# Performance work log

Hardware: AMD Instinct MI355X
Metric: run time of the kernel (lower is better)

The kernel has to match this reference:

```python
import jax, jax.numpy as jnp
import numpy as np

STDDEV = 8.0

def setup_inputs() -> dict:
    key = jax.random.key(0)
    k1, k2, k3, k4 = jax.random.split(key, 4)
    B, S, D, O = 32, 4096, 1024, 1024
    source_hidden_sequence = jax.random.normal(k1, (B, S, D), dtype=jnp.float32)
    target_hidden = jax.random.normal(k2, (B, D), dtype=jnp.float32)
    positions = jax.random.randint(k3, (B,), 0, S, dtype=jnp.int32)
    attention_weights = jax.random.normal(k4, (D + D, O), dtype=jnp.float32) * 0.02
    return {
        "source_hidden_sequence": source_hidden_sequence,
        "target_hidden": target_hidden,
        "positions": positions,
        "attention_weights": attention_weights,
    }

def reference(source_hidden_sequence, target_hidden, positions, attention_weights):
    # source_hidden_sequence: [B, S, D]; target_hidden: [B, D]; positions: [B]
    S = source_hidden_sequence.shape[1]
    # dot-product score per source position: [B, S]
    score = jnp.einsum('bsd,bd->bs', source_hidden_sequence, target_hidden)
    weights = jax.nn.softmax(score, axis=1)
    # Gaussian local-position decay centered at positions
    rel = jnp.arange(S, dtype=jnp.float32)[None, :] - positions.astype(jnp.float32)[:, None]  # [B, S]
    pos_w = jnp.exp(-(rel * rel) / (2.0 * STDDEV * STDDEV))
    weights = weights * pos_w
    # weighted sum over source sequence: [B, D]
    weighted = jnp.einsum('bsd,bs->bd', source_hidden_sequence, weights)
    combined = jnp.concatenate([target_hidden, weighted], axis=1)  # [B, 2D]
    return jnp.tanh(combined @ attention_weights)
```

## Files before the change

### kernel.cpp

```cpp
#include <hip/hip_runtime.h>

#define BB 32
#define SS 4096
#define DD 1024
#define OO 1024
#define KK 2048
#define RAD 64
#define NSPLIT 8

__global__ __launch_bounds__(256) void k_score(const float* __restrict__ src,
                                               const float* __restrict__ tgt,
                                               float* __restrict__ score) {
  const int b = blockIdx.y;
  const int wave = threadIdx.x >> 6;
  const int lane = threadIdx.x & 63;
  const int s_base = blockIdx.x * 16 + wave * 4;
  const float4* tv = (const float4*)(tgt + (size_t)b * DD);
  float4 q0 = tv[lane], q1 = tv[64 + lane], q2 = tv[128 + lane], q3 = tv[192 + lane];
  for (int i = 0; i < 4; ++i) {
    const int s = s_base + i;
    const float4* rv = (const float4*)(src + ((size_t)b * SS + s) * DD);
    float4 a0 = rv[lane], a1 = rv[64 + lane], a2 = rv[128 + lane], a3 = rv[192 + lane];
    float p = 0.f;
    p += a0.x*q0.x + a0.y*q0.y + a0.z*q0.z + a0.w*q0.w;
    p += a1.x*q1.x + a1.y*q1.y + a1.z*q1.z + a1.w*q1.w;
    p += a2.x*q2.x + a2.y*q2.y + a2.z*q2.z + a2.w*q2.w;
    p += a3.x*q3.x + a3.y*q3.y + a3.z*q3.z + a3.w*q3.w;
    for (int off = 32; off > 0; off >>= 1) p += __shfl_xor(p, off);
    if (lane == 0) score[(size_t)b * SS + s] = p;
  }
}

__global__ __launch_bounds__(256) void k_stats(const float* __restrict__ score,
                                               float* __restrict__ stats) {
  const int b = blockIdx.x;
  __shared__ float red[256];
  const float* sc = score + (size_t)b * SS;
  float m = -1e30f;
  for (int t = threadIdx.x; t < SS; t += 256) m = fmaxf(m, sc[t]);
  red[threadIdx.x] = m; __syncthreads();
  for (int off = 128; off > 0; off >>= 1) {
    if (threadIdx.x < off) red[threadIdx.x] = fmaxf(red[threadIdx.x], red[threadIdx.x + off]);
    __syncthreads();
  }
  m = red[0]; __syncthreads();
  float s = 0.f;
  for (int t = threadIdx.x; t < SS; t += 256) s += expf(sc[t] - m);
  red[threadIdx.x] = s; __syncthreads();
  for (int off = 128; off > 0; off >>= 1) {
    if (threadIdx.x < off) red[threadIdx.x] += red[threadIdx.x + off];
    __syncthreads();
  }
  if (threadIdx.x == 0) { stats[2 * b] = m; stats[2 * b + 1] = red[0]; }
}

__global__ __launch_bounds__(256) void k_weighted(const float* __restrict__ src,
                                                  const float* __restrict__ score,
                                                  const float* __restrict__ stats,
                                                  const int* __restrict__ pos,
                                                  float* __restrict__ partial) {
  const int b = blockIdx.y;
  const int split = blockIdx.x;
  const int p = pos[b];
  int w0 = p - RAD; if (w0 < 0) w0 = 0;
  int w1 = p + RAD + 1; if (w1 > SS) w1 = SS;
  const int len = w1 - w0;
  const int chunk = (len + NSPLIT - 1) / NSPLIT;
  int cs = w0 + split * chunk;
  int ce = cs + chunk; if (ce > w1) ce = w1;
  const float m = stats[2 * b];
  const float inv = 1.f / stats[2 * b + 1];
  const int t = threadIdx.x;
  float a0 = 0.f, a1 = 0.f, a2 = 0.f, a3 = 0.f;
  for (int s = cs; s < ce; ++s) {
    float rel = (float)(s - p);
    float w = expf(score[(size_t)b * SS + s] - m) * inv * expf(rel * rel * (-1.f / 128.f));
    float4 v = ((const float4*)(src + ((size_t)b * SS + s) * DD))[t];
    a0 += w * v.x; a1 += w * v.y; a2 += w * v.z; a3 += w * v.w;
  }
  float4* outp = (float4*)(partial + ((size_t)split * BB + b) * DD);
  outp[t] = make_float4(a0, a1, a2, a3);
}

__global__ __launch_bounds__(256) void k_out(const float* __restrict__ tgt,
                                             const float* __restrict__ partial,
                                             const float* __restrict__ W,
                                             float* __restrict__ out) {
  const int b = blockIdx.y;
  const int o0 = blockIdx.x * 128;
  __shared__ float c[KK];
  __shared__ float red[4][128];
  for (int k = threadIdx.x; k < KK; k += 256) {
    float v;
    if (k < DD) {
      v = tgt[(size_t)b * DD + k];
    } else {
      const int d = k - DD;
      v = 0.f;
      for (int pp = 0; pp < NSPLIT; ++pp) v += partial[((size_t)pp * BB + b) * DD + d];
    }
    c[k] = v;
  }
  __syncthreads();
  const int ks = threadIdx.x >> 6;
  const int ol = threadIdx.x & 63;
  float acc0 = 0.f, acc1 = 0.f;
  const float* wp = W + o0 + ol * 2;
  for (int k = ks * 512; k < ks * 512 + 512; ++k) {
    float2 wv = *(const float2*)(wp + (size_t)k * OO);
    float ck = c[k];
    acc0 += ck * wv.x; acc1 += ck * wv.y;
  }
  red[ks][ol * 2] = acc0;
  red[ks][ol * 2 + 1] = acc1;
  __syncthreads();
  if (threadIdx.x < 128) {
    float s = red[0][threadIdx.x] + red[1][threadIdx.x] + red[2][threadIdx.x] + red[3][threadIdx.x];
    out[(size_t)b * OO + o0 + threadIdx.x] = tanhf(s);
  }
}

extern "C" void kernel_launch(void* const* d_in, const int* in_sizes, int n_in,
                              void* d_out, int out_size, void* d_ws, size_t ws_size,
                              hipStream_t stream) {
  const float* src = (const float*)d_in[0];
  const float* tgt = (const float*)d_in[1];
  const int* pos   = (const int*)d_in[2];
  const float* W   = (const float*)d_in[3];
  float* out = (float*)d_out;

  float* ws      = (float*)d_ws;
  float* score   = ws;
  float* stats   = score + (size_t)BB * SS;
  float* partial = stats + 2 * BB;

  k_score   <<<dim3(SS / 16, BB), 256, 0, stream>>>(src, tgt, score);
  k_stats   <<<BB,                256, 0, stream>>>(score, stats);
  k_weighted<<<dim3(NSPLIT, BB),  256, 0, stream>>>(src, score, stats, pos, partial);
  k_out     <<<dim3(OO / 128, BB), 256, 0, stream>>>(tgt, partial, W, out);
}
```

Measured before the change: 718.5 us.

## Fuse per-block softmax stats into score kernel and batch row loads nontemporally

The score kernel now issues all 16 float4 loads for its four rows up front using nontemporal loads, reduces the four dot products together, and computes a per-block max and sum-of-exp in shared memory. The separate stats kernel, which reread the full score array, is replaced by a small combine kernel that merges the 256 block partials per batch with an online-softmax reduction. The intent is more memory-level parallelism on the dominant 512 MB streaming read and less work in the stats pass. The costs are more registers per thread, an extra block-level sync, and a new workspace region for block stats.

```diff
diff --git a/kernel.cpp b/kernel.cpp
--- a/kernel.cpp
+++ b/kernel.cpp
@@ -7,51 +7,103 @@
 #define KK 2048
 #define RAD 64
 #define NSPLIT 8
+#define NBLK (SS / 16)
+
+typedef float f4 __attribute__((ext_vector_type(4)));
+
+__device__ __forceinline__ float dot4(f4 a, f4 q) {
+  return a.x * q.x + a.y * q.y + a.z * q.z + a.w * q.w;
+}
 
 __global__ __launch_bounds__(256) void k_score(const float* __restrict__ src,
                                                const float* __restrict__ tgt,
-                                               float* __restrict__ score) {
+                                               float* __restrict__ score,
+                                               float* __restrict__ blkstats) {
   const int b = blockIdx.y;
   const int wave = threadIdx.x >> 6;
   const int lane = threadIdx.x & 63;
   const int s_base = blockIdx.x * 16 + wave * 4;
-  const float4* tv = (const float4*)(tgt + (size_t)b * DD);
-  float4 q0 = tv[lane], q1 = tv[64 + lane], q2 = tv[128 + lane], q3 = tv[192 + lane];
-  for (int i = 0; i < 4; ++i) {
-    const int s = s_base + i;
-    const float4* rv = (const float4*)(src + ((size_t)b * SS + s) * DD);
-    float4 a0 = rv[lane], a1 = rv[64 + lane], a2 = rv[128 + lane], a3 = rv[192 + lane];
-    float p = 0.f;
-    p += a0.x*q0.x + a0.y*q0.y + a0.z*q0.z + a0.w*q0.w;
-    p += a1.x*q1.x + a1.y*q1.y + a1.z*q1.z + a1.w*q1.w;
-    p += a2.x*q2.x + a2.y*q2.y + a2.z*q2.z + a2.w*q2.w;
-    p += a3.x*q3.x + a3.y*q3.y + a3.z*q3.z + a3.w*q3.w;
-    for (int off = 32; off > 0; off >>= 1) p += __shfl_xor(p, off);
-    if (lane == 0) score[(size_t)b * SS + s] = p;
+
+  const f4* tv = (const f4*)(tgt + (size_t)b * DD);
+  f4 q0 = tv[lane], q1 = tv[64 + lane], q2 = tv[128 + lane], q3 = tv[192 + lane];
+
+  const f4* r0 = (const f4*)(src + ((size_t)b * SS + s_base) * DD) + lane;
+  const f4* r1 = r0 + 256;
+  const f4* r2 = r0 + 512;
+  const f4* r3 = r0 + 768;
+
+  f4 a00 = __builtin_nontemporal_load(r0);
+  f4 a01 = __builtin_nontemporal_load(r0 + 64);
+  f4 a02 = __builtin_nontemporal_load(r0 + 128);
+  f4 a03 = __builtin_nontemporal_load(r0 + 192);
+  f4 a10 = __builtin_nontemporal_load(r1);
+  f4 a11 = __builtin_nontemporal_load(r1 + 64);
+  f4 a12 = __builtin_nontemporal_load(r1 + 128);
+  f4 a13 = __builtin_nontemporal_load(r1 + 192);
+  f4 a20 = __builtin_nontemporal_load(r2);
+  f4 a21 = __builtin_nontemporal_load(r2 + 64);
+  f4 a22 = __builtin_nontemporal_load(r2 + 128);
+  f4 a23 = __builtin_nontemporal_load(r2 + 192);
+  f4 a30 = __builtin_nontemporal_load(r3);
+  f4 a31 = __builtin_nontemporal_load(r3 + 64);
+  f4 a32 = __builtin_nontemporal_load(r3 + 128);
+  f4 a33 = __builtin_nontemporal_load(r3 + 192);
+
+  float p0 = (dot4(a00, q0) + dot4(a01, q1)) + (dot4(a02, q2) + dot4(a03, q3));
+  float p1 = (dot4(a10, q0) + dot4(a11, q1)) + (dot4(a12, q2) + dot4(a13, q3));
+  float p2 = (dot4(a20, q0) + dot4(a21, q1)) + (dot4(a22, q2) + dot4(a23, q3));
+  float p3 = (dot4(a30, q0) + dot4(a31, q1)) + (dot4(a32, q2) + dot4(a33, q3));
+
+  for (int off = 32; off > 0; off >>= 1) {
+    p0 += __shfl_xor(p0, off);
+    p1 += __shfl_xor(p1, off);
+    p2 += __shfl_xor(p2, off);
+    p3 += __shfl_xor(p3, off);
+  }
+
+  float sel = (lane == 0) ? p0 : ((lane == 1) ? p1 : ((lane == 2) ? p2 : p3));
+  if (lane < 4) score[(size_t)b * SS + s_base + lane] = sel;
+
+  __shared__ float rowv[16];
+  if (lane < 4) rowv[wave * 4 + lane] = sel;
+  __syncthreads();
+  if (threadIdx.x == 0) {
+    float m = rowv[0];
+    #pragma unroll
+    for (int i = 1; i < 16; ++i) m = fmaxf(m, rowv[i]);
+    float l = 0.f;
+    #pragma unroll
+    for (int i = 0; i < 16; ++i) l += expf(rowv[i] - m);
+    float* bs = blkstats + ((size_t)b * NBLK + blockIdx.x) * 2;
+    bs[0] = m; bs[1] = l;
   }
 }
 
-__global__ __launch_bounds__(256) void k_stats(const float* __restrict__ score,
-                                               float* __restrict__ stats) {
+__global__ __launch_bounds__(256) void k_combine(const float* __restrict__ blkstats,
+                                                 float* __restrict__ stats) {
   const int b = blockIdx.x;
-  __shared__ float red[256];
-  const float* sc = score + (size_t)b * SS;
-  float m = -1e30f;
-  for (int t = threadIdx.x; t < SS; t += 256) m = fmaxf(m, sc[t]);
-  red[threadIdx.x] = m; __syncthreads();
-  for (int off = 128; off > 0; off >>= 1) {
-    if (threadIdx.x < off) red[threadIdx.x] = fmaxf(red[threadIdx.x], red[threadIdx.x + off]);
-    __syncthreads();
+  const int wave = threadIdx.x >> 6;
+  const int lane = threadIdx.x & 63;
+  const float* bs = blkstats + ((size_t)b * NBLK + threadIdx.x) * 2;
+  float m = bs[0];
+  float l = bs[1];
+  for (int off = 32; off > 0; off >>= 1) {
+    float m2 = __shfl_xor(m, off);
+    float l2 = __shfl_xor(l, off);
+    float mm = fmaxf(m, m2);
+    l = l * expf(m - mm) + l2 * expf(m2 - mm);
+    m = mm;
   }
-  m = red[0]; __syncthreads();
-  float s = 0.f;
-  for (int t = threadIdx.x; t < SS; t += 256) s += expf(sc[t] - m);
-  red[threadIdx.x] = s; __syncthreads();
-  for (int off = 128; off > 0; off >>= 1) {
-    if (threadIdx.x < off) red[threadIdx.x] += red[threadIdx.x + off];
-    __syncthreads();
+  __shared__ float sm[4], sl[4];
+  if (lane == 0) { sm[wave] = m; sl[wave] = l; }
+  __syncthreads();
+  if (threadIdx.x == 0) {
+    float M = fmaxf(fmaxf(sm[0], sm[1]), fmaxf(sm[2], sm[3]));
+    float L = sl[0] * expf(sm[0] - M) + sl[1] * expf(sm[1] - M) +
+              sl[2] * expf(sm[2] - M) + sl[3] * expf(sm[3] - M);
+    stats[2 * b] = M;
+    stats[2 * b + 1] = L;
   }
-  if (threadIdx.x == 0) { stats[2 * b] = m; stats[2 * b + 1] = red[0]; }
 }
 
 __global__ __launch_bounds__(256) void k_weighted(const float* __restrict__ src,
@@ -75,11 +127,12 @@
   for (int s = cs; s < ce; ++s) {
     float rel = (float)(s - p);
     float w = expf(score[(size_t)b * SS + s] - m) * inv * expf(rel * rel * (-1.f / 128.f));
-    float4 v = ((const float4*)(src + ((size_t)b * SS + s) * DD))[t];
+    f4 v = ((const f4*)(src + ((size_t)b * SS + s) * DD))[t];
     a0 += w * v.x; a1 += w * v.y; a2 += w * v.z; a3 += w * v.w;
   }
-  float4* outp = (float4*)(partial + ((size_t)split * BB + b) * DD);
-  outp[t] = make_float4(a0, a1, a2, a3);
+  f4* outp = (f4*)(partial + ((size_t)split * BB + b) * DD);
+  f4 o; o.x = a0; o.y = a1; o.z = a2; o.w = a3;
+  outp[t] = o;
 }
 
 __global__ __launch_bounds__(256) void k_out(const float* __restrict__ tgt,
@@ -129,13 +182,14 @@
   const float* W   = (const float*)d_in[3];
   float* out = (float*)d_out;
 
-  float* ws      = (float*)d_ws;
-  float* score   = ws;
-  float* stats   = score + (size_t)BB * SS;
-  float* partial = stats + 2 * BB;
+  float* ws       = (float*)d_ws;
+  float* score    = ws;
+  float* stats    = score + (size_t)BB * SS;
+  float* partial  = stats + 2 * BB;
+  float* blkstats = partial + (size_t)NSPLIT * BB * DD;
 
-  k_score   <<<dim3(SS / 16, BB), 256, 0, stream>>>(src, tgt, score);
-  k_stats   <<<BB,                256, 0, stream>>>(score, stats);
+  k_score   <<<dim3(SS / 16, BB), 256, 0, stream>>>(src, tgt, score, blkstats);
+  k_combine <<<BB,                256, 0, stream>>>(blkstats, stats);
   k_weighted<<<dim3(NSPLIT, BB),  256, 0, stream>>>(src, score, stats, pos, partial);
   k_out     <<<dim3(OO / 128, BB), 256, 0, stream>>>(tgt, partial, W, out);
 }
```

After: 687.4 us. 4.3% less time.
